# Kernel optimization log

Hardware: AMD Instinct MI355X
Metric: run time of the kernel (lower is better)

Reference implementation:

```python
import jax, jax.numpy as jnp
import numpy as np

B, N, D_MEM, D_HID = 64, 65536, 1024, 1024


def setup_inputs() -> dict:
    key = jax.random.key(0)
    k1, k2, k3 = jax.random.split(key, 3)
    memory_bank = jax.random.normal(k1, (N, D_MEM), dtype=jnp.float32)
    decoder_state = jax.random.normal(k2, (B, D_HID), dtype=jnp.float32)
    # nn.Linear(memory_bank_size -> hidden_size, bias=False): weight [D_HID, D_MEM]
    W = jax.random.normal(k3, (D_HID, D_MEM), dtype=jnp.float32) / np.sqrt(D_MEM)
    # ragged tree sizes summing exactly to N (concrete, built on host)
    rng = np.random.default_rng(0)
    lens = rng.integers(512, 1536, size=B).astype(np.float64)
    lens = np.maximum(1, np.floor(lens * N / lens.sum()).astype(np.int64))
    lens[-1] += N - lens.sum()
    return {
        "memory_bank": memory_bank,
        "decoder_state": decoder_state,
        "W": W,
        "tree_node_num_lst": jnp.asarray(lens, dtype=jnp.int64),
    }


def reference(memory_bank, decoder_state, W, tree_node_num_lst):
    # segment id per node: tree index it belongs to (total_repeat_length keeps it jit-able)
    n_total = memory_bank.shape[0]
    batch = decoder_state.shape[0]
    seg = jnp.repeat(jnp.arange(batch), tree_node_num_lst, total_repeat_length=n_total)  # [N]
    # memory_project: one big GEMM instead of per-tree launches
    enc = memory_bank @ W.T                                  # [N, D_HID]
    # per-node score = <decoder_state[tree], enc[node]>
    scores = jnp.sum(enc * decoder_state[seg], axis=-1)      # [N]
    # segment (per-tree) stable softmax
    m = jax.ops.segment_max(scores, seg, num_segments=batch)  # [B]
    e = jnp.exp(scores - m[seg])                              # [N]
    z = jax.ops.segment_sum(e, seg, num_segments=batch)       # [B]
    attn = e / z[seg]                                         # [N]
    # context = attn-weighted sum of raw memory bank per tree
    context = jax.ops.segment_sum(attn[:, None] * memory_bank, seg, num_segments=batch)  # [B, D_MEM]
    return context
```

## Files before the change

### kernel.cpp

```cpp
#include <hip/hip_runtime.h>
#include <math.h>

#define B_TREES 64
#define N_NODES 65536
#define D 1024
#define D4 (D/4)

#define CHUNK 64
#define SUB 8
#define NSUB (CHUNK/SUB)
#define NCHUNK (N_NODES/CHUNK)
#define NSLOT (2*NCHUNK)
#define VZ 8

__device__ __forceinline__ void block_offsets(const int* __restrict__ lens32,
                                              int* __restrict__ soff,
                                              int tid, int lane) {
    if ((tid >> 6) == 0) {
        long long x32 = (long long)lens32[lane];
        long long tot = x32;
        #pragma unroll
        for (int o = 32; o > 0; o >>= 1) tot += __shfl_xor(tot, o, 64);
        int len = (tot == (long long)N_NODES) ? (int)x32
                                              : (int)(((const long long*)lens32)[lane]);
        int scan = len;
        #pragma unroll
        for (int o = 1; o < 64; o <<= 1) {
            int y = __shfl_up(scan, o, 64);
            if (lane >= o) scan += y;
        }
        soff[lane + 1] = scan;
        if (lane == 0) soff[0] = 0;
    }
}

__global__ __launch_bounds__(256) void v_kernel(const float* __restrict__ ds,
                                                const float* __restrict__ W,
                                                float* __restrict__ v_part) {
    const int m  = blockIdx.x * 256 + threadIdx.x;
    const int b0 = blockIdx.y * 4;
    const int z  = blockIdx.z;
    const int h0 = z * 128;
    float acc[4] = {0.f, 0.f, 0.f, 0.f};
    for (int h = h0; h < h0 + 128; ++h) {
        float wv = W[h * D + m];
        #pragma unroll
        for (int j = 0; j < 4; ++j)
            acc[j] += ds[(b0 + j) * D + h] * wv;
    }
    #pragma unroll
    for (int j = 0; j < 4; ++j)
        v_part[((size_t)(z * B_TREES + b0 + j)) * D + m] = acc[j];
}

__global__ __launch_bounds__(256, 4) void fused_kernel(
    const float4* __restrict__ mb, const float4* __restrict__ v_part,
    const int* __restrict__ lens32,
    float* __restrict__ m_arr, float* __restrict__ z_arr,
    int* __restrict__ seg_arr, float4* __restrict__ vec)
{
    __shared__ float red[2][4][SUB];
    __shared__ int   soff[B_TREES + 1];

    const int tid  = threadIdx.x;
    const int wave = tid >> 6;
    const int lane = tid & 63;
    const int c    = blockIdx.x;
    const int n0   = c * CHUNK;

    block_offsets(lens32, soff, tid, lane);
    __syncthreads();

    int lo = 0, hi = B_TREES - 1;
    while (lo < hi) { int mid = (lo + hi + 1) >> 1; if (soff[mid] <= n0) lo = mid; else hi = mid - 1; }
    const int sa   = lo;
    const int nxt  = soff[sa + 1];
    const int cutg = (nxt < n0 + CHUNK) ? nxt : 0x7fffffff;
    const bool two = (cutg != 0x7fffffff);

    float4 vA = make_float4(0.f, 0.f, 0.f, 0.f);
    #pragma unroll
    for (int z = 0; z < VZ; ++z) {
        const float4 t4 = v_part[(size_t)(z * B_TREES + sa) * D4 + tid];
        vA.x += t4.x; vA.y += t4.y; vA.z += t4.z; vA.w += t4.w;
    }
    float4 vB = vA;
    if (two) {
        vB = make_float4(0.f, 0.f, 0.f, 0.f);
        #pragma unroll
        for (int z = 0; z < VZ; ++z) {
            const float4 t4 = v_part[(size_t)(z * B_TREES + sa + 1) * D4 + tid];
            vB.x += t4.x; vB.y += t4.y; vB.z += t4.z; vB.w += t4.w;
        }
    }

    float  m0 = -INFINITY, z0 = 0.f, m1 = -INFINITY, z1 = 0.f;
    float4 a0 = make_float4(0.f, 0.f, 0.f, 0.f);
    float4 a1 = make_float4(0.f, 0.f, 0.f, 0.f);

    for (int st = 0; st < NSUB; ++st) {
        const int nb = n0 + st * SUB;

        float4 m4[SUB];
        #pragma unroll
        for (int k = 0; k < SUB; ++k)
            m4[k] = mb[(size_t)(nb + k) * D4 + tid];

        float p[SUB];
        if (nb + SUB <= cutg) {
            #pragma unroll
            for (int k = 0; k < SUB; ++k)
                p[k] = m4[k].x*vA.x + m4[k].y*vA.y + m4[k].z*vA.z + m4[k].w*vA.w;
        } else if (nb >= cutg) {
            #pragma unroll
            for (int k = 0; k < SUB; ++k)
                p[k] = m4[k].x*vB.x + m4[k].y*vB.y + m4[k].z*vB.z + m4[k].w*vB.w;
        } else {
            #pragma unroll
            for (int k = 0; k < SUB; ++k) {
                const float4 vk = (nb + k < cutg) ? vA : vB;
                p[k] = m4[k].x*vk.x + m4[k].y*vk.y + m4[k].z*vk.z + m4[k].w*vk.w;
            }
        }

        #pragma unroll
        for (int k = 0; k < SUB; ++k) {
            #pragma unroll
            for (int o = 32; o > 0; o >>= 1)
                p[k] += __shfl_xor(p[k], o, 64);
        }

        const int par = st & 1;
        if (lane == 0) {
            #pragma unroll
            for (int k = 0; k < SUB; ++k) red[par][wave][k] = p[k];
        }
        __syncthreads();
        float s[SUB];
        #pragma unroll
        for (int k = 0; k < SUB; ++k)
            s[k] = red[par][0][k] + red[par][1][k] + red[par][2][k] + red[par][3][k];

        #pragma unroll
        for (int k = 0; k < SUB; ++k) {
            const float sc_ = s[k];
            if (nb + k < cutg) {
                if (sc_ > m0) {
                    const float r = __expf(m0 - sc_);
                    z0 *= r; a0.x *= r; a0.y *= r; a0.z *= r; a0.w *= r;
                    m0 = sc_;
                }
                const float w = __expf(sc_ - m0);
                z0 += w;
                a0.x += w * m4[k].x; a0.y += w * m4[k].y;
                a0.z += w * m4[k].z; a0.w += w * m4[k].w;
            } else {
                if (sc_ > m1) {
                    const float r = __expf(m1 - sc_);
                    z1 *= r; a1.x *= r; a1.y *= r; a1.z *= r; a1.w *= r;
                    m1 = sc_;
                }
                const float w = __expf(sc_ - m1);
                z1 += w;
                a1.x += w * m4[k].x; a1.y += w * m4[k].y;
                a1.z += w * m4[k].z; a1.w += w * m4[k].w;
            }
        }
    }

    const int slot0 = 2 * c, slot1 = 2 * c + 1;
    vec[(size_t)slot0 * D4 + tid] = a0;
    if (tid == 0) { m_arr[slot0] = m0; z_arr[slot0] = z0; seg_arr[slot0] = sa; }
    if (two) {
        vec[(size_t)slot1 * D4 + tid] = a1;
        if (tid == 0) { m_arr[slot1] = m1; z_arr[slot1] = z1; seg_arr[slot1] = sa + 1; }
    } else if (tid == 0) {
        seg_arr[slot1] = -1;
    }
}

__global__ __launch_bounds__(256) void combine_kernel(
    const int* __restrict__ lens32, const float* __restrict__ m_arr,
    const float* __restrict__ z_arr, const int* __restrict__ seg_arr,
    const float4* __restrict__ vec, float4* __restrict__ out)
{
    __shared__ int soff[B_TREES + 1];
    const int t = threadIdx.x, lane = t & 63;
    block_offsets(lens32, soff, t, lane);
    __syncthreads();

    const int b  = blockIdx.x;
    const int s0 = soff[b], s1 = soff[b + 1];
    const int c0 = s0 / CHUNK, c1 = (s1 - 1) / CHUNK;

    float mseg = -INFINITY;
    for (int cc = c0; cc <= c1; ++cc) {
        #pragma unroll
        for (int j = 0; j < 2; ++j) {
            const int sl = 2 * cc + j;
            if (seg_arr[sl] == b) mseg = fmaxf(mseg, m_arr[sl]);
        }
    }
    float zseg = 0.f;
    float4 acc = make_float4(0.f, 0.f, 0.f, 0.f);
    for (int cc = c0; cc <= c1; ++cc) {
        #pragma unroll
        for (int j = 0; j < 2; ++j) {
            const int sl = 2 * cc + j;
            if (seg_arr[sl] == b) {
                const float sc = __expf(m_arr[sl] - mseg);
                zseg += sc * z_arr[sl];
                const float4 vv = vec[(size_t)sl * D4 + t];
                acc.x += sc * vv.x; acc.y += sc * vv.y;
                acc.z += sc * vv.z; acc.w += sc * vv.w;
            }
        }
    }
    const float inv = 1.f / zseg;
    acc.x *= inv; acc.y *= inv; acc.z *= inv; acc.w *= inv;
    out[(size_t)b * D4 + t] = acc;
}

extern "C" void kernel_launch(void* const* d_in, const int* in_sizes, int n_in,
                              void* d_out, int out_size, void* d_ws, size_t ws_size,
                              hipStream_t stream) {
    const float* mb   = (const float*)d_in[0];
    const float* ds   = (const float*)d_in[1];
    const float* W    = (const float*)d_in[2];
    const int*   lens = (const int*)d_in[3];
    float*       out  = (float*)d_out;

    char*  ws      = (char*)d_ws;
    float* v_part  = (float*)ws;
    float* m_arr   = (float*)(ws + (size_t)VZ * B_TREES * D * 4);
    float* z_arr   = m_arr + NSLOT;
    int*   seg_arr = (int*)(z_arr + NSLOT);
    float* vec     = (float*)((char*)(seg_arr + NSLOT));

    {
        dim3 grid(4, 16, VZ);
        v_kernel<<<grid, 256, 0, stream>>>(ds, W, v_part);
    }

    fused_kernel<<<NCHUNK, 256, 0, stream>>>(
        (const float4*)mb, (const float4*)v_part, lens,
        m_arr, z_arr, seg_arr, (float4*)vec);

    combine_kernel<<<B_TREES, 256, 0, stream>>>(
        lens, m_arr, z_arr, seg_arr, (const float4*)vec, (float4*)out);
}
```

Before: 399.5 us.

## Double-buffer memory bank loads and use transpose-style wave reduction

Prefetches the next 8-row sub-block of the memory bank into registers while the current one is processed, using ping-pong buffers across an unrolled loop. The first block's load is issued before the offsets scan so it overlaps that setup. The eight per-row wave reductions are replaced by a butterfly reduce-scatter that needs far fewer shuffles, with lanes 0-7 each writing one score. Occupancy hint drops from 4 to 3 blocks per CU to make room for the extra registers, which may reduce latency hiding across blocks.

```diff
diff --git a/kernel.cpp b/kernel.cpp
--- a/kernel.cpp
+++ b/kernel.cpp
@@ -53,7 +53,108 @@
         v_part[((size_t)(z * B_TREES + b0 + j)) * D + m] = acc[j];
 }
 
-__global__ __launch_bounds__(256, 4) void fused_kernel(
+struct FusedState {
+    float  m0, z0, m1, z1;
+    float4 a0, a1;
+};
+
+__device__ __forceinline__ void fused_body(
+    const float4* __restrict__ mb, float4 (&CUR)[SUB], float4 (&NXT)[SUB],
+    int ST, int n0, int cutg, const float4& vA, const float4& vB,
+    int tid, int wave, int lane, float (*red)[4][SUB], FusedState& S)
+{
+    const int nb = n0 + ST * SUB;
+
+    if (ST + 1 < NSUB) {
+        const int nb2 = nb + SUB;
+        #pragma unroll
+        for (int k = 0; k < SUB; ++k)
+            NXT[k] = mb[(size_t)(nb2 + k) * D4 + tid];
+    }
+
+    float p[SUB];
+    if (nb + SUB <= cutg) {
+        #pragma unroll
+        for (int k = 0; k < SUB; ++k)
+            p[k] = CUR[k].x*vA.x + CUR[k].y*vA.y + CUR[k].z*vA.z + CUR[k].w*vA.w;
+    } else if (nb >= cutg) {
+        #pragma unroll
+        for (int k = 0; k < SUB; ++k)
+            p[k] = CUR[k].x*vB.x + CUR[k].y*vB.y + CUR[k].z*vB.z + CUR[k].w*vB.w;
+    } else {
+        #pragma unroll
+        for (int k = 0; k < SUB; ++k) {
+            const float4 vk = (nb + k < cutg) ? vA : vB;
+            p[k] = CUR[k].x*vk.x + CUR[k].y*vk.y + CUR[k].z*vk.z + CUR[k].w*vk.w;
+        }
+    }
+
+    float r01, r23, r45, r67, q0, q1, r;
+    {
+        const bool h1 = (lane & 1) != 0;
+        float keep, send;
+        keep = h1 ? p[1] : p[0]; send = h1 ? p[0] : p[1];
+        r01 = keep + __shfl_xor(send, 1, 64);
+        keep = h1 ? p[3] : p[2]; send = h1 ? p[2] : p[3];
+        r23 = keep + __shfl_xor(send, 1, 64);
+        keep = h1 ? p[5] : p[4]; send = h1 ? p[4] : p[5];
+        r45 = keep + __shfl_xor(send, 1, 64);
+        keep = h1 ? p[7] : p[6]; send = h1 ? p[6] : p[7];
+        r67 = keep + __shfl_xor(send, 1, 64);
+    }
+    {
+        const bool h2 = (lane & 2) != 0;
+        float keep, send;
+        keep = h2 ? r23 : r01; send = h2 ? r01 : r23;
+        q0 = keep + __shfl_xor(send, 2, 64);
+        keep = h2 ? r67 : r45; send = h2 ? r45 : r67;
+        q1 = keep + __shfl_xor(send, 2, 64);
+    }
+    {
+        const bool h4 = (lane & 4) != 0;
+        float keep = h4 ? q1 : q0, send = h4 ? q0 : q1;
+        r = keep + __shfl_xor(send, 4, 64);
+    }
+    r += __shfl_xor(r, 8, 64);
+    r += __shfl_xor(r, 16, 64);
+    r += __shfl_xor(r, 32, 64);
+
+    const int par = ST & 1;
+    if (lane < 8) red[par][wave][lane] = r;
+    __syncthreads();
+    float s_[SUB];
+    #pragma unroll
+    for (int k = 0; k < SUB; ++k)
+        s_[k] = red[par][0][k] + red[par][1][k] + red[par][2][k] + red[par][3][k];
+
+    #pragma unroll
+    for (int k = 0; k < SUB; ++k) {
+        const float sc_ = s_[k];
+        if (nb + k < cutg) {
+            if (sc_ > S.m0) {
+                const float rr = __expf(S.m0 - sc_);
+                S.z0 *= rr; S.a0.x *= rr; S.a0.y *= rr; S.a0.z *= rr; S.a0.w *= rr;
+                S.m0 = sc_;
+            }
+            const float w = __expf(sc_ - S.m0);
+            S.z0 += w;
+            S.a0.x += w * CUR[k].x; S.a0.y += w * CUR[k].y;
+            S.a0.z += w * CUR[k].z; S.a0.w += w * CUR[k].w;
+        } else {
+            if (sc_ > S.m1) {
+                const float rr = __expf(S.m1 - sc_);
+                S.z1 *= rr; S.a1.x *= rr; S.a1.y *= rr; S.a1.z *= rr; S.a1.w *= rr;
+                S.m1 = sc_;
+            }
+            const float w = __expf(sc_ - S.m1);
+            S.z1 += w;
+            S.a1.x += w * CUR[k].x; S.a1.y += w * CUR[k].y;
+            S.a1.z += w * CUR[k].z; S.a1.w += w * CUR[k].w;
+        }
+    }
+}
+
+__global__ __launch_bounds__(256, 3) void fused_kernel(
     const float4* __restrict__ mb, const float4* __restrict__ v_part,
     const int* __restrict__ lens32,
     float* __restrict__ m_arr, float* __restrict__ z_arr,
@@ -68,6 +169,11 @@
     const int c    = blockIdx.x;
     const int n0   = c * CHUNK;
 
+    float4 bufA[SUB], bufB[SUB];
+    #pragma unroll
+    for (int k = 0; k < SUB; ++k)
+        bufA[k] = mb[(size_t)(n0 + k) * D4 + tid];
+
     block_offsets(lens32, soff, tid, lane);
     __syncthreads();
 
@@ -94,86 +200,23 @@
         }
     }
 
-    float  m0 = -INFINITY, z0 = 0.f, m1 = -INFINITY, z1 = 0.f;
-    float4 a0 = make_float4(0.f, 0.f, 0.f, 0.f);
-    float4 a1 = make_float4(0.f, 0.f, 0.f, 0.f);
-
-    for (int st = 0; st < NSUB; ++st) {
-        const int nb = n0 + st * SUB;
-
-        float4 m4[SUB];
-        #pragma unroll
-        for (int k = 0; k < SUB; ++k)
-            m4[k] = mb[(size_t)(nb + k) * D4 + tid];
-
-        float p[SUB];
-        if (nb + SUB <= cutg) {
-            #pragma unroll
-            for (int k = 0; k < SUB; ++k)
-                p[k] = m4[k].x*vA.x + m4[k].y*vA.y + m4[k].z*vA.z + m4[k].w*vA.w;
-        } else if (nb >= cutg) {
-            #pragma unroll
-            for (int k = 0; k < SUB; ++k)
-                p[k] = m4[k].x*vB.x + m4[k].y*vB.y + m4[k].z*vB.z + m4[k].w*vB.w;
-        } else {
-            #pragma unroll
-            for (int k = 0; k < SUB; ++k) {
-                const float4 vk = (nb + k < cutg) ? vA : vB;
-                p[k] = m4[k].x*vk.x + m4[k].y*vk.y + m4[k].z*vk.z + m4[k].w*vk.w;
-            }
-        }
-
-        #pragma unroll
-        for (int k = 0; k < SUB; ++k) {
-            #pragma unroll
-            for (int o = 32; o > 0; o >>= 1)
-                p[k] += __shfl_xor(p[k], o, 64);
-        }
-
-        const int par = st & 1;
-        if (lane == 0) {
-            #pragma unroll
-            for (int k = 0; k < SUB; ++k) red[par][wave][k] = p[k];
-        }
-        __syncthreads();
-        float s[SUB];
-        #pragma unroll
-        for (int k = 0; k < SUB; ++k)
-            s[k] = red[par][0][k] + red[par][1][k] + red[par][2][k] + red[par][3][k];
-
-        #pragma unroll
-        for (int k = 0; k < SUB; ++k) {
-            const float sc_ = s[k];
-            if (nb + k < cutg) {
-                if (sc_ > m0) {
-                    const float r = __expf(m0 - sc_);
-                    z0 *= r; a0.x *= r; a0.y *= r; a0.z *= r; a0.w *= r;
-                    m0 = sc_;
-                }
-                const float w = __expf(sc_ - m0);
-                z0 += w;
-                a0.x += w * m4[k].x; a0.y += w * m4[k].y;
-                a0.z += w * m4[k].z; a0.w += w * m4[k].w;
-            } else {
-                if (sc_ > m1) {
-                    const float r = __expf(m1 - sc_);
-                    z1 *= r; a1.x *= r; a1.y *= r; a1.z *= r; a1.w *= r;
-                    m1 = sc_;
-                }
-                const float w = __expf(sc_ - m1);
-                z1 += w;
-                a1.x += w * m4[k].x; a1.y += w * m4[k].y;
-                a1.z += w * m4[k].z; a1.w += w * m4[k].w;
-            }
-        }
+    FusedState S;
+    S.m0 = -INFINITY; S.z0 = 0.f; S.m1 = -INFINITY; S.z1 = 0.f;
+    S.a0 = make_float4(0.f, 0.f, 0.f, 0.f);
+    S.a1 = make_float4(0.f, 0.f, 0.f, 0.f);
+
+    #pragma unroll
+    for (int st = 0; st < NSUB; st += 2) {
+        fused_body(mb, bufA, bufB, st,     n0, cutg, vA, vB, tid, wave, lane, red, S);
+        fused_body(mb, bufB, bufA, st + 1, n0, cutg, vA, vB, tid, wave, lane, red, S);
     }
 
     const int slot0 = 2 * c, slot1 = 2 * c + 1;
-    vec[(size_t)slot0 * D4 + tid] = a0;
-    if (tid == 0) { m_arr[slot0] = m0; z_arr[slot0] = z0; seg_arr[slot0] = sa; }
+    vec[(size_t)slot0 * D4 + tid] = S.a0;
+    if (tid == 0) { m_arr[slot0] = S.m0; z_arr[slot0] = S.z0; seg_arr[slot0] = sa; }
     if (two) {
-        vec[(size_t)slot1 * D4 + tid] = a1;
-        if (tid == 0) { m_arr[slot1] = m1; z_arr[slot1] = z1; seg_arr[slot1] = sa + 1; }
+        vec[(size_t)slot1 * D4 + tid] = S.a1;
+        if (tid == 0) { m_arr[slot1] = S.m1; z_arr[slot1] = S.z1; seg_arr[slot1] = sa + 1; }
     } else if (tid == 0) {
         seg_arr[slot1] = -1;
     }
```

New measurement: 385.7 us. 1.04x faster.
